# Performance work log

Hardware: AMD Instinct MI355X
Metric: run time of the kernel (lower is better)

Reference implementation:

```python
import jax, jax.numpy as jnp
import numpy as np

N_NODES = 50000
N_EDGES = 800000


def _inv_sqrt_deg(idx, n):
    deg = jax.ops.segment_sum(jnp.ones(idx.shape, jnp.float32), idx, num_segments=n)
    return jnp.where(deg > 0, deg ** -0.5, 0.0)


def graph_conv(x, W, b, src, dst, norm_src, norm_dst):
    # DGL GraphConv, norm='both': D_dst^{-1/2} A D_src^{-1/2} X W + b
    # Apply weight before aggregation (out_feats < in_feats in both layers).
    h = (x * norm_src[:, None]) @ W            # [N, out]
    m = h[src]                                  # gather per-edge messages [E, out]
    agg = jax.ops.segment_sum(m, dst, num_segments=x.shape[0])
    return agg * norm_dst[:, None] + b


def setup_inputs() -> dict:
    key = jax.random.key(0)
    ks = jax.random.split(key, 6)
    x = jax.random.normal(ks[0], (N_NODES, 512), jnp.float32)
    W1 = jax.random.normal(ks[1], (512, 128), jnp.float32) * (512 ** -0.5)
    b1 = jnp.zeros((128,), jnp.float32)
    W2 = jax.random.normal(ks[2], (128, 40), jnp.float32) * (128 ** -0.5)
    b2 = jnp.zeros((40,), jnp.float32)
    src = jax.random.randint(ks[3], (N_EDGES,), 0, N_NODES, jnp.int32)
    dst = jax.random.randint(ks[4], (N_EDGES,), 0, N_NODES, jnp.int32)
    return {"x": x, "W1": W1, "b1": b1, "W2": W2, "b2": b2, "src": src, "dst": dst}


def reference(x, W1, b1, W2, b2, src, dst):
    n = x.shape[0]
    norm_src = _inv_sqrt_deg(src, n)  # out-degree based src norm
    norm_dst = _inv_sqrt_deg(dst, n)  # in-degree based dst norm
    h = graph_conv(x, W1, b1, src, dst, norm_src, norm_dst)
    h = jax.nn.relu(h)
    h = graph_conv(h, W2, b2, src, dst, norm_src, norm_dst)
    return h
```

## Files before the change

kernel.cpp:

```cpp
#include <hip/hip_runtime.h>
#include <hip/hip_bf16.h>

#define F0 512
#define F1 128
#define F2 40

#define NRP 12800
#define G_SL 64

typedef __attribute__((ext_vector_type(8))) short bf16x8;
typedef __attribute__((ext_vector_type(4))) float f32x4;

__device__ inline ushort f2bf(float f) {
    union { float f; uint u; } v; v.f = f;
    uint u = v.u;
    uint r = u + 0x7fffu + ((u >> 16) & 1u);
    return (ushort)(r >> 16);
}

#define CVT2(dst, a, b) { __hip_bfloat162 _t2 = __float22bfloat162_rn(make_float2(a, b)); __builtin_memcpy(&dst, &_t2, 4); }

__global__ __launch_bounds__(1024)
void hist_kernel(const int* __restrict__ src, const int* __restrict__ dst,
                 uchar* __restrict__ Gsrc, uchar* __restrict__ Gdst,
                 const float* __restrict__ W1, ushort* __restrict__ Wt, int n, int E) {
    if (blockIdx.x < (F0 * F1) / 1024) {
        int idx = blockIdx.x * 1024 + threadIdx.x;
        int k = idx >> 7, nn = idx & 127;
        Wt[nn * F0 + k] = f2bf(W1[idx]);
    }
    __shared__ uint cs[NRP / 2];
    __shared__ uint cd[NRP / 2];
    const int p = blockIdx.x / G_SL;
    const int g = blockIdx.x % G_SL;
    const int base = p * NRP;
    for (int i = threadIdx.x; i < NRP / 2; i += 1024) { cs[i] = 0; cd[i] = 0; }
    __syncthreads();
    const int Epg = (E + G_SL - 1) / G_SL;
    const int e0 = g * Epg;
    const int e1 = min(E, e0 + Epg);
    for (int i = e0 + (int)threadIdx.x; i < e1; i += 1024) {
        int s = src[i], d = dst[i];
        unsigned so = (unsigned)(s - base);
        unsigned dd = (unsigned)(d - base);
        if (so < (unsigned)NRP) atomicAdd(&cs[so >> 1], 1u << ((so & 1) * 16));
        if (dd < (unsigned)NRP) atomicAdd(&cd[dd >> 1], 1u << ((dd & 1) * 16));
    }
    __syncthreads();
    const int lim = min(NRP, n - base);
    for (int i = threadIdx.x; i < lim; i += 1024) {
        uint pcs = cs[i >> 1], pcd = cd[i >> 1];
        int sh = (i & 1) * 16;
        Gsrc[(size_t)g * n + base + i] = (uchar)((pcs >> sh) & 0xffu);
        Gdst[(size_t)g * n + base + i] = (uchar)((pcd >> sh) & 0xffu);
    }
}

__global__ __launch_bounds__(256)
void scanA_kernel(const uchar* __restrict__ Gsrc, const uchar* __restrict__ Gdst,
                  float* __restrict__ norm_src, float* __restrict__ norm_dst,
                  int* __restrict__ row_off, int* __restrict__ bsum, int n) {
    __shared__ int sm[256];
    int i = blockIdx.x * 256 + threadIdx.x;
    int s = 0, d = 0;
    if (i < n) {
#pragma unroll
        for (int g = 0; g < G_SL; g++) {
            s += Gsrc[(size_t)g * n + i];
            d += Gdst[(size_t)g * n + i];
        }
        norm_src[i] = s > 0 ? rsqrtf((float)s) : 0.f;
        norm_dst[i] = d > 0 ? rsqrtf((float)d) : 0.f;
    }
    sm[threadIdx.x] = (i < n) ? d : 0;
    __syncthreads();
    for (int off = 1; off < 256; off <<= 1) {
        int t = (threadIdx.x >= (unsigned)off) ? sm[threadIdx.x - off] : 0;
        __syncthreads();
        sm[threadIdx.x] += t;
        __syncthreads();
    }
    if (i < n) row_off[i + 1] = sm[threadIdx.x];
    if (threadIdx.x == 255) bsum[blockIdx.x] = sm[255];
}

__global__ __launch_bounds__(256)
void finalize_kernel(int* __restrict__ row_off, const int* __restrict__ bsum,
                     const uchar* __restrict__ Gdst, int* __restrict__ Goff, int n) {
    __shared__ int sm[256];
    const int b = blockIdx.x;
    const int t = threadIdx.x;
    sm[t] = (t < b) ? bsum[t] : 0;
    __syncthreads();
#pragma unroll
    for (int off = 128; off > 0; off >>= 1) {
        if (t < off) sm[t] += sm[t + off];
        __syncthreads();
    }
    const int excl = sm[0];
    const int v = b * 256 + t;
    if (v >= n) return;
    int raw = row_off[v];
    int start = excl + ((t == 0) ? 0 : raw);
    if (v == n - 1) {
        int rawn = row_off[n];
        row_off[n] = excl + rawn;
    }
    row_off[v] = start;
    int run = start;
#pragma unroll
    for (int g = 0; g < G_SL; g++) {
        size_t idx = (size_t)g * n + v;
        Goff[idx] = run;
        run += Gdst[idx];
    }
}

#define BM 64
#define NKT 4

union SmemU {
    int cur[NRP];
    char Al[2][32768];
};

#define ISSUE4(kt, buf) {                                                              \
    __builtin_amdgcn_global_load_lds(                                                  \
        (const __attribute__((address_space(1))) void*)(gs0 + (kt) * 128),             \
        (__attribute__((address_space(3))) void*)(&smu.Al[buf][tid * 16]),             \
        16, 0, 0);                                                                     \
    __builtin_amdgcn_global_load_lds(                                                  \
        (const __attribute__((address_space(1))) void*)(gs1 + (kt) * 128),             \
        (__attribute__((address_space(3))) void*)(&smu.Al[buf][8192 + tid * 16]),      \
        16, 0, 0);                                                                     \
    __builtin_amdgcn_global_load_lds(                                                  \
        (const __attribute__((address_space(1))) void*)(gs2 + (kt) * 128),             \
        (__attribute__((address_space(3))) void*)(&smu.Al[buf][16384 + tid * 16]),     \
        16, 0, 0);                                                                     \
    __builtin_amdgcn_global_load_lds(                                                  \
        (const __attribute__((address_space(1))) void*)(gs3 + (kt) * 128),             \
        (__attribute__((address_space(3))) void*)(&smu.Al[buf][24576 + tid * 16]),     \
        16, 0, 0); }

#define LOADB4(kt, arr) {                                                              \
    arr[0] = *reinterpret_cast<const bf16x8*>(bp + (kt) * 128 + 0);                    \
    arr[1] = *reinterpret_cast<const bf16x8*>(bp + (kt) * 128 + 32);                   \
    arr[2] = *reinterpret_cast<const bf16x8*>(bp + (kt) * 128 + 64);                   \
    arr[3] = *reinterpret_cast<const bf16x8*>(bp + (kt) * 128 + 96); }

#define MKFRAG(dst, mi, kk, bufp) {                                                    \
    const int _row = (mi) * 16 + l15;                                                  \
    const char* _pr = (bufp) + _row * 512;                                             \
    const int _sw = (l15 & 7) << 2;                                                    \
    float4 _pa = *reinterpret_cast<const float4*>(_pr + ((((kk) * 8 + 2 * lq + 0) ^ _sw) << 4)); \
    float4 _pb = *reinterpret_cast<const float4*>(_pr + ((((kk) * 8 + 2 * lq + 1) ^ _sw) << 4)); \
    union { uint u[4]; bf16x8 v; } _pk;                                                \
    CVT2(_pk.u[0], _pa.x, _pa.y); CVT2(_pk.u[1], _pa.z, _pa.w);                        \
    CVT2(_pk.u[2], _pb.x, _pb.y); CVT2(_pk.u[3], _pb.z, _pb.w);                        \
    dst = _pk.v; }

#define COMPUTE16(buf, barr) {                                                         \
    const char* _bp = &smu.Al[buf][0];                                                 \
    _Pragma("unroll")                                                                  \
    for (int kk = 0; kk < 4; ++kk) {                                                   \
        bf16x8 _a0, _a1, _a2, _a3;                                                     \
        MKFRAG(_a0, 0, kk, _bp); MKFRAG(_a1, 1, kk, _bp);                              \
        MKFRAG(_a2, 2, kk, _bp); MKFRAG(_a3, 3, kk, _bp);                              \
        acc[0] = __builtin_amdgcn_mfma_f32_16x16x32_bf16(_a0, barr[kk], acc[0], 0, 0, 0); \
        acc[1] = __builtin_amdgcn_mfma_f32_16x16x32_bf16(_a1, barr[kk], acc[1], 0, 0, 0); \
        acc[2] = __builtin_amdgcn_mfma_f32_16x16x32_bf16(_a2, barr[kk], acc[2], 0, 0, 0); \
        acc[3] = __builtin_amdgcn_mfma_f32_16x16x32_bf16(_a3, barr[kk], acc[3], 0, 0, 0); \
    } }

__global__ __launch_bounds__(512)
void place_gemm1_fused(const int* __restrict__ src, const int* __restrict__ dst,
                       const int* __restrict__ Goff, int* __restrict__ edge_src,
                       const float* __restrict__ x, const ushort* __restrict__ Wt,
                       const float* __restrict__ norm_src, ushort* __restrict__ h1g,
                       int n, int E, int ngemm) {
    __shared__ __align__(16) SmemU smu;
    const int tid = threadIdx.x;

    if (blockIdx.x >= ngemm) {
        const int pb = blockIdx.x - ngemm;
        const int p = pb / G_SL;
        const int g = pb % G_SL;
        const int base = p * NRP;
        const int lim = min(NRP, n - base);
        for (int i = tid; i < lim; i += 512)
            smu.cur[i] = Goff[(size_t)g * n + base + i];
        __syncthreads();
        const int Epg = (E + G_SL - 1) / G_SL;
        const int e0 = g * Epg;
        const int e1 = min(E, e0 + Epg);
        for (int i = e0 + tid; i < e1; i += 512) {
            int d = dst[i];
            unsigned dd = (unsigned)(d - base);
            if (dd < (unsigned)lim) {
                int pos = atomicAdd(&smu.cur[dd], 1);
                edge_src[pos] = src[i];
            }
        }
        return;
    }

    const int lane = tid & 63;
    const int w = tid >> 6;
    const int l15 = lane & 15;
    const int lq = lane >> 4;
    const int bm = blockIdx.x * BM;

    const int st_sub = tid >> 5;
    const int slot = tid & 31;
    const int sslot = slot ^ ((st_sub & 7) << 2);
    int g0 = bm + 0 * 16 + st_sub;  if (g0 >= n) g0 = n - 1;
    int g1 = bm + 1 * 16 + st_sub;  if (g1 >= n) g1 = n - 1;
    int g2 = bm + 2 * 16 + st_sub;  if (g2 >= n) g2 = n - 1;
    int g3 = bm + 3 * 16 + st_sub;  if (g3 >= n) g3 = n - 1;
    const float* gs0 = x + (size_t)g0 * F0 + sslot * 4;
    const float* gs1 = x + (size_t)g1 * F0 + sslot * 4;
    const float* gs2 = x + (size_t)g2 * F0 + sslot * 4;
    const float* gs3 = x + (size_t)g3 * F0 + sslot * 4;

    const ushort* bp = Wt + (size_t)(w * 16 + l15) * F0 + lq * 8;

    f32x4 acc[4] = {};
    bf16x8 bcur[4], bnxt[4];

    ISSUE4(0, 0);
    LOADB4(0, bcur);
    __syncthreads();

    for (int kt = 0; kt < NKT; ++kt) {
        const int cb = kt & 1;
        if (kt < NKT - 1) {
            ISSUE4(kt + 1, cb ^ 1);
            LOADB4(kt + 1, bnxt);
        }
        COMPUTE16(cb, bcur);
#pragma unroll
        for (int j = 0; j < 4; ++j) bcur[j] = bnxt[j];
        if (kt < NKT - 1) __syncthreads();
    }

#pragma unroll
    for (int mi = 0; mi < 4; mi++) {
        int rbase = bm + mi * 16 + lq * 4;
#pragma unroll
        for (int r = 0; r < 4; r++) {
            int row = rbase + r;
            if (row < n) {
                float ns = norm_src[row];
                h1g[(size_t)row * F1 + w * 16 + l15] = f2bf(acc[mi][r] * ns);
            }
        }
    }
}

__global__ __launch_bounds__(256)
void agg1_kernel(const ushort* __restrict__ h1g, const int* __restrict__ row_off,
                 const int* __restrict__ edge_src, const float* __restrict__ norm_dst,
                 const float* __restrict__ b1, ushort* __restrict__ h1, int n) {
    int wid = (blockIdx.x * blockDim.x + threadIdx.x) >> 6;
    int lane = threadIdx.x & 63;
    if (wid >= n) return;
    int beg = row_off[wid], end = row_off[wid + 1];
    float a0 = 0.f, a1 = 0.f;
    int e = beg;
    for (; e + 7 < end; e += 8) {
        int s[8];
#pragma unroll
        for (int j = 0; j < 8; j++) s[j] = edge_src[e + j];
        uint v[8];
#pragma unroll
        for (int j = 0; j < 8; j++)
            v[j] = *reinterpret_cast<const uint*>(&h1g[(size_t)s[j] * F1 + lane * 2]);
#pragma unroll
        for (int j = 0; j < 8; j++) {
            a0 += __uint_as_float(v[j] << 16);
            a1 += __uint_as_float(v[j] & 0xffff0000u);
        }
    }
    for (; e < end; ++e) {
        int s = edge_src[e];
        uint v = *reinterpret_cast<const uint*>(&h1g[(size_t)s * F1 + lane * 2]);
        a0 += __uint_as_float(v << 16);
        a1 += __uint_as_float(v & 0xffff0000u);
    }
    float nd = norm_dst[wid];
    float o0 = fmaxf(a0 * nd + b1[lane * 2 + 0], 0.f);
    float o1 = fmaxf(a1 * nd + b1[lane * 2 + 1], 0.f);
    __hip_bfloat162 p2 = __float22bfloat162_rn(make_float2(o0, o1));
    uint pu; __builtin_memcpy(&pu, &p2, 4);
    *reinterpret_cast<uint*>(&h1[(size_t)wid * F1 + lane * 2]) = pu;
}

__global__ __launch_bounds__(256)
void gemm2_kernel(const ushort* __restrict__ h1, const float* __restrict__ W2,
                  const float* __restrict__ norm_src, ushort* __restrict__ h2g, int n) {
    __shared__ __align__(16) float W2s[F1][F2];
    for (int i = threadIdx.x; i < F1 * F2; i += 256)
        W2s[i / F2][i % F2] = W2[i];
    __syncthreads();
    int node = blockIdx.x * 256 + threadIdx.x;
    if (node >= n) return;
    float nrm = norm_src[node];
    f32x4 acc4[10] = {};
    const ushort* row = &h1[(size_t)node * F1];
    for (int kc = 0; kc < 16; kc++) {
        uint4 u = *reinterpret_cast<const uint4*>(&row[kc * 8]);
        uint uu[4] = {u.x, u.y, u.z, u.w};
        float f[8];
#pragma unroll
        for (int i = 0; i < 4; i++) {
            f[2 * i + 0] = __uint_as_float(uu[i] << 16);
            f[2 * i + 1] = __uint_as_float(uu[i] & 0xffff0000u);
        }
#pragma unroll
        for (int j = 0; j < 8; j++) {
#pragma unroll
            for (int c4 = 0; c4 < 10; c4++) {
                f32x4 wv = *reinterpret_cast<const f32x4*>(&W2s[kc * 8 + j][c4 * 4]);
                acc4[c4] += f[j] * wv;
            }
        }
    }
    ushort* orow = &h2g[(size_t)node * F2];
#pragma unroll
    for (int c4 = 0; c4 < 10; c4++) {
        f32x4 o = acc4[c4] * nrm;
        __hip_bfloat162 pa = __float22bfloat162_rn(make_float2(o[0], o[1]));
        __hip_bfloat162 pb = __float22bfloat162_rn(make_float2(o[2], o[3]));
        uint2 pk;
        __builtin_memcpy(&pk.x, &pa, 4);
        __builtin_memcpy(&pk.y, &pb, 4);
        *reinterpret_cast<uint2*>(&orow[c4 * 4]) = pk;
    }
}

__global__ __launch_bounds__(256)
void agg2_kernel(const ushort* __restrict__ h2g, const int* __restrict__ row_off,
                 const int* __restrict__ edge_src, const float* __restrict__ norm_dst,
                 const float* __restrict__ b2, float* __restrict__ out, int n) {
    int wid = (blockIdx.x * blockDim.x + threadIdx.x) >> 6;
    int lane = threadIdx.x & 63;
    if (wid >= n) return;
    int beg = row_off[wid], end = row_off[wid + 1];
    float a0 = 0.f, a1 = 0.f;
    int e = beg;
    const bool act = lane < 20;
    for (; e + 7 < end; e += 8) {
        int s[8];
#pragma unroll
        for (int j = 0; j < 8; j++) s[j] = edge_src[e + j];
        if (act) {
            uint v[8];
#pragma unroll
            for (int j = 0; j < 8; j++)
                v[j] = *reinterpret_cast<const uint*>(&h2g[(size_t)s[j] * F2 + lane * 2]);
#pragma unroll
            for (int j = 0; j < 8; j++) {
                a0 += __uint_as_float(v[j] << 16);
                a1 += __uint_as_float(v[j] & 0xffff0000u);
            }
        }
    }
    for (; e < end; ++e) {
        int s = edge_src[e];
        if (act) {
            uint v = *reinterpret_cast<const uint*>(&h2g[(size_t)s * F2 + lane * 2]);
            a0 += __uint_as_float(v << 16);
            a1 += __uint_as_float(v & 0xffff0000u);
        }
    }
    if (act) {
        float nd = norm_dst[wid];
        float o0 = a0 * nd + b2[lane * 2 + 0];
        float o1 = a1 * nd + b2[lane * 2 + 1];
        *reinterpret_cast<float2*>(&out[(size_t)wid * F2 + lane * 2]) = make_float2(o0, o1);
    }
}

extern "C" void kernel_launch(void* const* d_in, const int* in_sizes, int n_in,
                              void* d_out, int out_size, void* d_ws, size_t ws_size,
                              hipStream_t stream) {
    const float* x  = (const float*)d_in[0];
    const float* W1 = (const float*)d_in[1];
    const float* b1 = (const float*)d_in[2];
    const float* W2 = (const float*)d_in[3];
    const float* b2 = (const float*)d_in[4];
    const int* src  = (const int*)d_in[5];
    const int* dst  = (const int*)d_in[6];
    float* out = (float*)d_out;

    const int n = in_sizes[0] / F0;
    const int E = in_sizes[5];
    const int nb = (n + 255) / 256;
    const int P = (n + NRP - 1) / NRP;
    const int ngemm = (n + BM - 1) / BM;

    char* ws = (char*)d_ws;
    auto alloc = [&](size_t bytes) -> char* {
        char* p = ws;
        ws += (bytes + 255) & ~(size_t)255;
        return p;
    };
    int* row_off   = (int*)alloc((size_t)(n + 1) * 4);
    int* bsum      = (int*)alloc(256 * 4);
    int* edge_srcs = (int*)alloc((size_t)E * 4);
    float* norm_src_d = (float*)alloc((size_t)n * 4);
    float* norm_dst_d = (float*)alloc((size_t)n * 4);
    ushort* W1t = (ushort*)alloc((size_t)F1 * F0 * 2);
    ushort* h1g = (ushort*)alloc((size_t)n * F1 * 2);
    ushort* h1  = (ushort*)alloc((size_t)n * F1 * 2);
    ushort* h2g = h1g;

    uchar* Gsrc = (uchar*)h1g;
    uchar* Gdst = Gsrc + (size_t)G_SL * n;
    int* Goff = (int*)h1;

    hist_kernel<<<P * G_SL, 1024, 0, stream>>>(src, dst, Gsrc, Gdst, W1, W1t, n, E);
    scanA_kernel<<<nb, 256, 0, stream>>>(Gsrc, Gdst, norm_src_d, norm_dst_d, row_off, bsum, n);
    finalize_kernel<<<nb, 256, 0, stream>>>(row_off, bsum, Gdst, Goff, n);
    place_gemm1_fused<<<ngemm + P * G_SL, 512, 0, stream>>>(
        src, dst, Goff, edge_srcs, x, W1t, norm_src_d, h1g, n, E, ngemm);
    agg1_kernel<<<(n + 3) / 4, 256, 0, stream>>>(h1g, row_off, edge_srcs, norm_dst_d, b1, h1, n);
    gemm2_kernel<<<(n + 255) / 256, 256, 0, stream>>>(h1, W2, norm_src_d, h2g, n);
    agg2_kernel<<<(n + 3) / 4, 256, 0, stream>>>(h2g, row_off, edge_srcs, norm_dst_d, b2, out, n);
}
```

Baseline: 181.7 us.

## Split GEMM1 across histogram and placement kernels, move src norm into aggregation

```diff
diff --git a/kernel.cpp b/kernel.cpp
--- a/kernel.cpp
+++ b/kernel.cpp
@@ -20,109 +20,15 @@
 
 #define CVT2(dst, a, b) { __hip_bfloat162 _t2 = __float22bfloat162_rn(make_float2(a, b)); __builtin_memcpy(&dst, &_t2, 4); }
 
-__global__ __launch_bounds__(1024)
-void hist_kernel(const int* __restrict__ src, const int* __restrict__ dst,
-                 uchar* __restrict__ Gsrc, uchar* __restrict__ Gdst,
-                 const float* __restrict__ W1, ushort* __restrict__ Wt, int n, int E) {
-    if (blockIdx.x < (F0 * F1) / 1024) {
-        int idx = blockIdx.x * 1024 + threadIdx.x;
-        int k = idx >> 7, nn = idx & 127;
-        Wt[nn * F0 + k] = f2bf(W1[idx]);
-    }
-    __shared__ uint cs[NRP / 2];
-    __shared__ uint cd[NRP / 2];
-    const int p = blockIdx.x / G_SL;
-    const int g = blockIdx.x % G_SL;
-    const int base = p * NRP;
-    for (int i = threadIdx.x; i < NRP / 2; i += 1024) { cs[i] = 0; cd[i] = 0; }
-    __syncthreads();
-    const int Epg = (E + G_SL - 1) / G_SL;
-    const int e0 = g * Epg;
-    const int e1 = min(E, e0 + Epg);
-    for (int i = e0 + (int)threadIdx.x; i < e1; i += 1024) {
-        int s = src[i], d = dst[i];
-        unsigned so = (unsigned)(s - base);
-        unsigned dd = (unsigned)(d - base);
-        if (so < (unsigned)NRP) atomicAdd(&cs[so >> 1], 1u << ((so & 1) * 16));
-        if (dd < (unsigned)NRP) atomicAdd(&cd[dd >> 1], 1u << ((dd & 1) * 16));
-    }
-    __syncthreads();
-    const int lim = min(NRP, n - base);
-    for (int i = threadIdx.x; i < lim; i += 1024) {
-        uint pcs = cs[i >> 1], pcd = cd[i >> 1];
-        int sh = (i & 1) * 16;
-        Gsrc[(size_t)g * n + base + i] = (uchar)((pcs >> sh) & 0xffu);
-        Gdst[(size_t)g * n + base + i] = (uchar)((pcd >> sh) & 0xffu);
-    }
-}
-
-__global__ __launch_bounds__(256)
-void scanA_kernel(const uchar* __restrict__ Gsrc, const uchar* __restrict__ Gdst,
-                  float* __restrict__ norm_src, float* __restrict__ norm_dst,
-                  int* __restrict__ row_off, int* __restrict__ bsum, int n) {
-    __shared__ int sm[256];
-    int i = blockIdx.x * 256 + threadIdx.x;
-    int s = 0, d = 0;
-    if (i < n) {
-#pragma unroll
-        for (int g = 0; g < G_SL; g++) {
-            s += Gsrc[(size_t)g * n + i];
-            d += Gdst[(size_t)g * n + i];
-        }
-        norm_src[i] = s > 0 ? rsqrtf((float)s) : 0.f;
-        norm_dst[i] = d > 0 ? rsqrtf((float)d) : 0.f;
-    }
-    sm[threadIdx.x] = (i < n) ? d : 0;
-    __syncthreads();
-    for (int off = 1; off < 256; off <<= 1) {
-        int t = (threadIdx.x >= (unsigned)off) ? sm[threadIdx.x - off] : 0;
-        __syncthreads();
-        sm[threadIdx.x] += t;
-        __syncthreads();
-    }
-    if (i < n) row_off[i + 1] = sm[threadIdx.x];
-    if (threadIdx.x == 255) bsum[blockIdx.x] = sm[255];
-}
-
-__global__ __launch_bounds__(256)
-void finalize_kernel(int* __restrict__ row_off, const int* __restrict__ bsum,
-                     const uchar* __restrict__ Gdst, int* __restrict__ Goff, int n) {
-    __shared__ int sm[256];
-    const int b = blockIdx.x;
-    const int t = threadIdx.x;
-    sm[t] = (t < b) ? bsum[t] : 0;
-    __syncthreads();
-#pragma unroll
-    for (int off = 128; off > 0; off >>= 1) {
-        if (t < off) sm[t] += sm[t + off];
-        __syncthreads();
-    }
-    const int excl = sm[0];
-    const int v = b * 256 + t;
-    if (v >= n) return;
-    int raw = row_off[v];
-    int start = excl + ((t == 0) ? 0 : raw);
-    if (v == n - 1) {
-        int rawn = row_off[n];
-        row_off[n] = excl + rawn;
-    }
-    row_off[v] = start;
-    int run = start;
-#pragma unroll
-    for (int g = 0; g < G_SL; g++) {
-        size_t idx = (size_t)g * n + v;
-        Goff[idx] = run;
-        run += Gdst[idx];
-    }
+__global__ __launch_bounds__(256)
+void wconv_kernel(const float* __restrict__ W1, ushort* __restrict__ Wt) {
+    int idx = blockIdx.x * 256 + threadIdx.x;
+    int k = idx >> 7, nn = idx & 127;
+    Wt[nn * F0 + k] = f2bf(W1[idx]);
 }
 
 #define BM 64
 #define NKT 4
-
-union SmemU {
-    int cur[NRP];
-    char Al[2][32768];
-};
 
 #define ISSUE4(kt, buf) {                                                              \
     __builtin_amdgcn_global_load_lds(                                                  \
@@ -172,17 +78,169 @@
         acc[3] = __builtin_amdgcn_mfma_f32_16x16x32_bf16(_a3, barr[kk], acc[3], 0, 0, 0); \
     } }
 
+#define GEMM_BODY(row_block)                                                           \
+    const int lane = tid & 63;                                                         \
+    const int w = tid >> 6;                                                            \
+    const int l15 = lane & 15;                                                         \
+    const int lq = lane >> 4;                                                          \
+    const int bm = (row_block) * BM;                                                   \
+    const int st_sub = tid >> 5;                                                       \
+    const int slot = tid & 31;                                                         \
+    const int sslot = slot ^ ((st_sub & 7) << 2);                                      \
+    int g0 = bm + 0 * 16 + st_sub;  if (g0 >= n) g0 = n - 1;                           \
+    int g1 = bm + 1 * 16 + st_sub;  if (g1 >= n) g1 = n - 1;                           \
+    int g2 = bm + 2 * 16 + st_sub;  if (g2 >= n) g2 = n - 1;                           \
+    int g3 = bm + 3 * 16 + st_sub;  if (g3 >= n) g3 = n - 1;                           \
+    const float* gs0 = x + (size_t)g0 * F0 + sslot * 4;                                \
+    const float* gs1 = x + (size_t)g1 * F0 + sslot * 4;                                \
+    const float* gs2 = x + (size_t)g2 * F0 + sslot * 4;                                \
+    const float* gs3 = x + (size_t)g3 * F0 + sslot * 4;                                \
+    const ushort* bp = Wt + (size_t)(w * 16 + l15) * F0 + lq * 8;                      \
+    f32x4 acc[4] = {};                                                                 \
+    bf16x8 bcur[4], bnxt[4];                                                           \
+    ISSUE4(0, 0);                                                                      \
+    LOADB4(0, bcur);                                                                   \
+    __syncthreads();                                                                   \
+    for (int kt = 0; kt < NKT; ++kt) {                                                 \
+        const int cb = kt & 1;                                                         \
+        if (kt < NKT - 1) {                                                            \
+            ISSUE4(kt + 1, cb ^ 1);                                                    \
+            LOADB4(kt + 1, bnxt);                                                      \
+        }                                                                              \
+        COMPUTE16(cb, bcur);                                                           \
+        _Pragma("unroll")                                                              \
+        for (int j = 0; j < 4; ++j) bcur[j] = bnxt[j];                                 \
+        if (kt < NKT - 1) __syncthreads();                                             \
+    }                                                                                  \
+    _Pragma("unroll")                                                                  \
+    for (int mi = 0; mi < 4; mi++) {                                                   \
+        int rbase = bm + mi * 16 + lq * 4;                                             \
+        _Pragma("unroll")                                                              \
+        for (int r = 0; r < 4; r++) {                                                  \
+            int row = rbase + r;                                                       \
+            if (row < n)                                                               \
+                h1g[(size_t)row * F1 + w * 16 + l15] = f2bf(acc[mi][r]);               \
+        }                                                                              \
+    }
+
+union SmemHG {
+    struct { uint cs[NRP / 2]; uint cd[NRP / 2]; } h;
+    char Al[2][32768];
+};
+
+__global__ __launch_bounds__(512)
+void hist_gemm1_fused(const int* __restrict__ src, const int* __restrict__ dst,
+                      uchar* __restrict__ Gsrc, uchar* __restrict__ Gdst,
+                      const float* __restrict__ x, const ushort* __restrict__ Wt,
+                      ushort* __restrict__ h1g, int n, int E, int ngemm_a) {
+    __shared__ __align__(16) SmemHG smu;
+    const int tid = threadIdx.x;
+
+    if (blockIdx.x >= ngemm_a) {
+        const int pb = blockIdx.x - ngemm_a;
+        const int p = pb / G_SL;
+        const int g = pb % G_SL;
+        const int base = p * NRP;
+        for (int i = tid; i < NRP / 2; i += 512) { smu.h.cs[i] = 0; smu.h.cd[i] = 0; }
+        __syncthreads();
+        const int Epg = (E + G_SL - 1) / G_SL;
+        const int e0 = g * Epg;
+        const int e1 = min(E, e0 + Epg);
+        for (int i = e0 + tid; i < e1; i += 512) {
+            int s = src[i], d = dst[i];
+            unsigned so = (unsigned)(s - base);
+            unsigned dd = (unsigned)(d - base);
+            if (so < (unsigned)NRP) atomicAdd(&smu.h.cs[so >> 1], 1u << ((so & 1) * 16));
+            if (dd < (unsigned)NRP) atomicAdd(&smu.h.cd[dd >> 1], 1u << ((dd & 1) * 16));
+        }
+        __syncthreads();
+        const int lim = min(NRP, n - base);
+        for (int i = tid; i < lim; i += 512) {
+            uint pcs = smu.h.cs[i >> 1], pcd = smu.h.cd[i >> 1];
+            int sh = (i & 1) * 16;
+            Gsrc[(size_t)g * n + base + i] = (uchar)((pcs >> sh) & 0xffu);
+            Gdst[(size_t)g * n + base + i] = (uchar)((pcd >> sh) & 0xffu);
+        }
+        return;
+    }
+    GEMM_BODY((int)blockIdx.x)
+}
+
+__global__ __launch_bounds__(256)
+void scanA_kernel(const uchar* __restrict__ Gsrc, const uchar* __restrict__ Gdst,
+                  float* __restrict__ norm_src, float* __restrict__ norm_dst,
+                  int* __restrict__ row_off, int* __restrict__ bsum, int n) {
+    __shared__ int sm[256];
+    int i = blockIdx.x * 256 + threadIdx.x;
+    int s = 0, d = 0;
+    if (i < n) {
+#pragma unroll
+        for (int g = 0; g < G_SL; g++) {
+            s += Gsrc[(size_t)g * n + i];
+            d += Gdst[(size_t)g * n + i];
+        }
+        norm_src[i] = s > 0 ? rsqrtf((float)s) : 0.f;
+        norm_dst[i] = d > 0 ? rsqrtf((float)d) : 0.f;
+    }
+    sm[threadIdx.x] = (i < n) ? d : 0;
+    __syncthreads();
+    for (int off = 1; off < 256; off <<= 1) {
+        int t = (threadIdx.x >= (unsigned)off) ? sm[threadIdx.x - off] : 0;
+        __syncthreads();
+        sm[threadIdx.x] += t;
+        __syncthreads();
+    }
+    if (i < n) row_off[i + 1] = sm[threadIdx.x];
+    if (threadIdx.x == 255) bsum[blockIdx.x] = sm[255];
+}
+
+__global__ __launch_bounds__(256)
+void finalize_kernel(int* __restrict__ row_off, const int* __restrict__ bsum,
+                     const uchar* __restrict__ Gdst, int* __restrict__ Goff, int n) {
+    __shared__ int sm[256];
+    const int b = blockIdx.x;
+    const int t = threadIdx.x;
+    sm[t] = (t < b) ? bsum[t] : 0;
+    __syncthreads();
+#pragma unroll
+    for (int off = 128; off > 0; off >>= 1) {
+        if (t < off) sm[t] += sm[t + off];
+        __syncthreads();
+    }
+    const int excl = sm[0];
+    const int v = b * 256 + t;
+    if (v >= n) return;
+    int raw = row_off[v];
+    int start = excl + ((t == 0) ? 0 : raw);
+    if (v == n - 1) {
+        int rawn = row_off[n];
+        row_off[n] = excl + rawn;
+    }
+    row_off[v] = start;
+    int run = start;
+#pragma unroll
+    for (int g = 0; g < G_SL; g++) {
+        size_t idx = (size_t)g * n + v;
+        Goff[idx] = run;
+        run += Gdst[idx];
+    }
+}
+
+union SmemPG {
+    int cur[NRP];
+    char Al[2][32768];
+};
+
 __global__ __launch_bounds__(512)
 void place_gemm1_fused(const int* __restrict__ src, const int* __restrict__ dst,
                        const int* __restrict__ Goff, int* __restrict__ edge_src,
                        const float* __restrict__ x, const ushort* __restrict__ Wt,
-                       const float* __restrict__ norm_src, ushort* __restrict__ h1g,
-                       int n, int E, int ngemm) {
-    __shared__ __align__(16) SmemU smu;
+                       ushort* __restrict__ h1g, int n, int E, int ngemm_b, int row_base) {
+    __shared__ __align__(16) SmemPG smu;
     const int tid = threadIdx.x;
 
-    if (blockIdx.x >= ngemm) {
-        const int pb = blockIdx.x - ngemm;
+    if (blockIdx.x >= ngemm_b) {
+        const int pb = blockIdx.x - ngemm_b;
         const int p = pb / G_SL;
         const int g = pb % G_SL;
         const int base = p * NRP;
@@ -203,64 +261,14 @@
         }
         return;
     }
-
-    const int lane = tid & 63;
-    const int w = tid >> 6;
-    const int l15 = lane & 15;
-    const int lq = lane >> 4;
-    const int bm = blockIdx.x * BM;
-
-    const int st_sub = tid >> 5;
-    const int slot = tid & 31;
-    const int sslot = slot ^ ((st_sub & 7) << 2);
-    int g0 = bm + 0 * 16 + st_sub;  if (g0 >= n) g0 = n - 1;
-    int g1 = bm + 1 * 16 + st_sub;  if (g1 >= n) g1 = n - 1;
-    int g2 = bm + 2 * 16 + st_sub;  if (g2 >= n) g2 = n - 1;
-    int g3 = bm + 3 * 16 + st_sub;  if (g3 >= n) g3 = n - 1;
-    const float* gs0 = x + (size_t)g0 * F0 + sslot * 4;
-    const float* gs1 = x + (size_t)g1 * F0 + sslot * 4;
-    const float* gs2 = x + (size_t)g2 * F0 + sslot * 4;
-    const float* gs3 = x + (size_t)g3 * F0 + sslot * 4;
-
-    const ushort* bp = Wt + (size_t)(w * 16 + l15) * F0 + lq * 8;
-
-    f32x4 acc[4] = {};
-    bf16x8 bcur[4], bnxt[4];
-
-    ISSUE4(0, 0);
-    LOADB4(0, bcur);
-    __syncthreads();
-
-    for (int kt = 0; kt < NKT; ++kt) {
-        const int cb = kt & 1;
-        if (kt < NKT - 1) {
-            ISSUE4(kt + 1, cb ^ 1);
-            LOADB4(kt + 1, bnxt);
-        }
-        COMPUTE16(cb, bcur);
-#pragma unroll
-        for (int j = 0; j < 4; ++j) bcur[j] = bnxt[j];
-        if (kt < NKT - 1) __syncthreads();
-    }
-
-#pragma unroll
-    for (int mi = 0; mi < 4; mi++) {
-        int rbase = bm + mi * 16 + lq * 4;
-#pragma unroll
-        for (int r = 0; r < 4; r++) {
-            int row = rbase + r;
-            if (row < n) {
-                float ns = norm_src[row];
-                h1g[(size_t)row * F1 + w * 16 + l15] = f2bf(acc[mi][r] * ns);
-            }
-        }
-    }
+    GEMM_BODY(row_base + (int)blockIdx.x)
 }
 
 __global__ __launch_bounds__(256)
 void agg1_kernel(const ushort* __restrict__ h1g, const int* __restrict__ row_off,
-                 const int* __restrict__ edge_src, const float* __restrict__ norm_dst,
-                 const float* __restrict__ b1, ushort* __restrict__ h1, int n) {
+                 const int* __restrict__ edge_src, const float* __restrict__ norm_src,
+                 const float* __restrict__ norm_dst, const float* __restrict__ b1,
+                 ushort* __restrict__ h1, int n) {
     int wid = (blockIdx.x * blockDim.x + threadIdx.x) >> 6;
     int lane = threadIdx.x & 63;
     if (wid >= n) return;
@@ -272,20 +280,24 @@
 #pragma unroll
         for (int j = 0; j < 8; j++) s[j] = edge_src[e + j];
         uint v[8];
-#pragma unroll
-        for (int j = 0; j < 8; j++)
+        float ns[8];
+#pragma unroll
+        for (int j = 0; j < 8; j++) {
             v[j] = *reinterpret_cast<const uint*>(&h1g[(size_t)s[j] * F1 + lane * 2]);
+            ns[j] = norm_src[s[j]];
+        }
 #pragma unroll
         for (int j = 0; j < 8; j++) {
-            a0 += __uint_as_float(v[j] << 16);
-            a1 += __uint_as_float(v[j] & 0xffff0000u);
+            a0 += ns[j] * __uint_as_float(v[j] << 16);
+            a1 += ns[j] * __uint_as_float(v[j] & 0xffff0000u);
         }
     }
     for (; e < end; ++e) {
         int s = edge_src[e];
         uint v = *reinterpret_cast<const uint*>(&h1g[(size_t)s * F1 + lane * 2]);
-        a0 += __uint_as_float(v << 16);
-        a1 += __uint_as_float(v & 0xffff0000u);
+        float ns = norm_src[s];
+        a0 += ns * __uint_as_float(v << 16);
+        a1 += ns * __uint_as_float(v & 0xffff0000u);
     }
     float nd = norm_dst[wid];
     float o0 = fmaxf(a0 * nd + b1[lane * 2 + 0], 0.f);
@@ -398,6 +410,8 @@
     const int nb = (n + 255) / 256;
     const int P = (n + NRP - 1) / NRP;
     const int ngemm = (n + BM - 1) / BM;
+    const int ngemm_a = (ngemm + 1) / 2;
+    const int ngemm_b = ngemm - ngemm_a;
 
     char* ws = (char*)d_ws;
     auto alloc = [&](size_t bytes) -> char* {
@@ -411,20 +425,22 @@
     float* norm_src_d = (float*)alloc((size_t)n * 4);
     float* norm_dst_d = (float*)alloc((size_t)n * 4);
     ushort* W1t = (ushort*)alloc((size_t)F1 * F0 * 2);
+    uchar* Gsrc = (uchar*)alloc((size_t)G_SL * n);
+    uchar* Gdst = (uchar*)alloc((size_t)G_SL * n);
     ushort* h1g = (ushort*)alloc((size_t)n * F1 * 2);
     ushort* h1  = (ushort*)alloc((size_t)n * F1 * 2);
     ushort* h2g = h1g;
-
-    uchar* Gsrc = (uchar*)h1g;
-    uchar* Gdst = Gsrc + (size_t)G_SL * n;
     int* Goff = (int*)h1;
 
-    hist_kernel<<<P * G_SL, 1024, 0, stream>>>(src, dst, Gsrc, Gdst, W1, W1t, n, E);
+    wconv_kernel<<<(F0 * F1) / 256, 256, 0, stream>>>(W1, W1t);
+    hist_gemm1_fused<<<ngemm_a + P * G_SL, 512, 0, stream>>>(
+        src, dst, Gsrc, Gdst, x, W1t, h1g, n, E, ngemm_a);
     scanA_kernel<<<nb, 256, 0, stream>>>(Gsrc, Gdst, norm_src_d, norm_dst_d, row_off, bsum, n);
     finalize_kernel<<<nb, 256, 0, stream>>>(row_off, bsum, Gdst, Goff, n);
-    place_gemm1_fused<<<ngemm + P * G_SL, 512, 0, stream>>>(
-        src, dst, Goff, edge_srcs, x, W1t, norm_src_d, h1g, n, E, ngemm);
-    agg1_kernel<<<(n + 3) / 4, 256, 0, stream>>>(h1g, row_off, edge_srcs, norm_dst_d, b1, h1, n);
+    place_gemm1_fused<<<ngemm_b + P * G_SL, 512, 0, stream>>>(
+        src, dst, Goff, edge_srcs, x, W1t, h1g, n, E, ngemm_b, ngemm_a);
+    agg1_kernel<<<(n + 3) / 4, 256, 0, stream>>>(h1g, row_off, edge_srcs, norm_src_d,
+                                                 norm_dst_d, b1, h1, n);
     gemm2_kernel<<<(n + 255) / 256, 256, 0, stream>>>(h1, W2, norm_src_d, h2g, n);
     agg2_kernel<<<(n + 3) / 4, 256, 0, stream>>>(h2g, row_off, edge_srcs, norm_dst_d, b2, out, n);
 }
```

Measured after the change: 185.0 us. About the same (+1.8%).
